# Optimization experiments

Measured on AMD Instinct MI355X. Metric: run time of the kernel, lower is better.

The kernel has to match this reference:

```python
import jax, jax.numpy as jnp
import numpy as np

NUM_OBJECTS = 6          # self.NUM_OBJECTS
SCORE_THRESH = 1e-4      # self.score_tresh
NMS_THRESHS = jnp.asarray(np.arange(0.001, 1.0, 0.1), dtype=jnp.float32)  # 10 thresholds
K_CAND = 1024            # fixed-shape cap on (proposal,class) candidates per image
CLASS_OFFSET = 4096.0    # > max image coord; batched_nms per-class offset trick


def _iou_matrix(b):
    # b: [K,4] xyxy -> [K,K] IoU
    x1, y1, x2, y2 = b[:, 0], b[:, 1], b[:, 2], b[:, 3]
    area = (x2 - x1) * (y2 - y1)
    iw = jnp.clip(jnp.minimum(x2[:, None], x2[None, :]) - jnp.maximum(x1[:, None], x1[None, :]), 0.0)
    ih = jnp.clip(jnp.minimum(y2[:, None], y2[None, :]) - jnp.maximum(y1[:, None], y1[None, :]), 0.0)
    inter = iw * ih
    union = area[:, None] + area[None, :] - inter
    return jnp.where(union > 0, inter / union, 0.0)


def _greedy_nms(iou, valid, thresh):
    # candidates are pre-sorted by descending score; sequential greedy suppression
    K = valid.shape[0]
    ar = jnp.arange(K)
    def body(i, keep):
        sup = keep[i] & (iou[i] > thresh) & (ar > i)
        return keep & ~sup
    return jax.lax.fori_loop(0, K, body, valid)


def _per_image(logits, boxes, feats, hw):
    # logits [N,81], boxes [N,80,4], feats [N,2048], hw [2] (h,w)
    C = boxes.shape[1]
    probs = jax.nn.softmax(logits, axis=-1)[:, :C]          # drop background class
    h = hw[0].astype(boxes.dtype)
    w = hw[1].astype(boxes.dtype)
    b = jnp.stack([jnp.clip(boxes[..., 0], 0.0, w),         # clip to image
                   jnp.clip(boxes[..., 1], 0.0, h),
                   jnp.clip(boxes[..., 2], 0.0, w),
                   jnp.clip(boxes[..., 3], 0.0, h)], axis=-1)
    scores = probs.reshape(-1)                              # [N*C]
    vals, idx = jax.lax.top_k(jnp.where(scores > SCORE_THRESH, scores, -1.0), K_CAND)
    cand_valid = vals > SCORE_THRESH
    cb = b.reshape(-1, 4)[idx]                              # [K,4]
    cls = (idx % C).astype(boxes.dtype)
    prop = idx // C                                         # proposal row index
    iou = _iou_matrix(cb + cls[:, None] * CLASS_OFFSET)     # per-class NMS via offsets
    keeps = jax.vmap(lambda t: _greedy_nms(iou, cand_valid, t))(NMS_THRESHS)  # [T,K]
    counts = keeps.sum(axis=1)
    # torch loop: break at first (smallest) thresh yielding len(ids)==6, i.e. >=6 kept
    ok = counts >= NUM_OBJECTS
    t_sel = jnp.where(jnp.any(ok), jnp.argmax(ok), NMS_THRESHS.shape[0] - 1)
    keep = keeps[t_sel]
    _, top = jax.lax.top_k(jnp.where(keep, vals, -jnp.inf), NUM_OBJECTS)
    ids = prop[top]                                         # [6]
    return feats[ids].T                                     # [2048, 6] (permute(1,0))


def _forward(cls_logits, boxes, feature_pooled, image_hw):
    return jax.vmap(_per_image)(cls_logits, boxes, feature_pooled, image_hw)  # [B,2048,6]


def setup_inputs() -> dict:
    key = jax.random.key(0)
    k1, k2, k3, k4, k5 = jax.random.split(key, 5)
    B, N, C, D = 8, 1000, 80, 2048
    cls_logits = jax.random.normal(k1, (B, N, C + 1), dtype=jnp.float32)
    ctr = jax.random.uniform(k2, (B, N, C, 2), minval=0.0, maxval=800.0)
    sz = jax.random.uniform(k3, (B, N, C, 2), minval=8.0, maxval=200.0)
    boxes = jnp.concatenate([ctr - sz * 0.5, ctr + sz * 0.5], axis=-1).astype(jnp.float32)
    feature_pooled = jax.random.normal(k4, (B, N, D), dtype=jnp.float32)
    image_hw = jax.random.randint(k5, (B, 2), 600, 800, dtype=jnp.int32)
    return {"cls_logits": cls_logits, "boxes": boxes,
            "feature_pooled": feature_pooled, "image_hw": image_hw}


def reference(cls_logits, boxes, feature_pooled, image_hw):
    return _forward(cls_logits, boxes, feature_pooled, image_hw)
```

## Files before the change

### kernel.cpp

```cpp
#include <hip/hip_runtime.h>
#include <cmath>
#include <cstdint>

#define NB 8
#define NPROP 1000
#define NCLS 80
#define NLOG 81
#define KCAND 1024
#define NTH 10
#define DFEAT 2048
#define NOBJ 6
#define NSCORE (NPROP*NCLS)
#define HBLK 8
#define HCHUNK (NSCORE/HBLK)
#define PCHUNK (NPROP/HBLK)
#define CCAP 64

constexpr size_t OFF_SCORES = 0;
constexpr size_t SZ_SCORES  = (size_t)NB * NSCORE * 4;
constexpr size_t OFF_LISTA  = OFF_SCORES + SZ_SCORES;
constexpr size_t SZ_LISTA   = (size_t)NB * 20 * KCAND * 8;
constexpr size_t OFF_H1     = OFF_LISTA;
constexpr size_t OFF_H2     = OFF_H1 + (size_t)NB * HBLK * 2048 * 4;
constexpr size_t OFF_PIV    = OFF_H2 + (size_t)NB * HBLK * 2048 * 4;
constexpr size_t OFF_CBUF   = OFF_PIV + (size_t)NB * 8 * 4;
constexpr size_t OFF_CANDK  = OFF_LISTA + SZ_LISTA;
constexpr size_t SZ_CANDK   = (size_t)NB * KCAND * 8;
constexpr size_t OFF_CX1    = OFF_CANDK + SZ_CANDK;
constexpr size_t SZ_CARR    = (size_t)NB * KCAND * 4;
constexpr size_t OFF_CY1    = OFF_CX1 + SZ_CARR;
constexpr size_t OFF_CX2    = OFF_CY1 + SZ_CARR;
constexpr size_t OFF_CY2    = OFF_CX2 + SZ_CARR;
constexpr size_t OFF_CAREA  = OFF_CY2 + SZ_CARR;
constexpr size_t OFF_CPROP  = OFF_CAREA + SZ_CARR;
constexpr size_t OFF_VALIDW = OFF_CPROP + SZ_CARR;
constexpr size_t SZ_VALIDW  = (size_t)NB * 16 * 8;
constexpr size_t OFF_CCNT   = OFF_VALIDW + SZ_VALIDW;
constexpr size_t OFF_CLIST  = OFF_CCNT + (size_t)NB * NCLS * 4;
constexpr size_t OFF_KEEPS  = OFF_CLIST + (size_t)NB * NCLS * CCAP * 4;
constexpr size_t SZ_KEEPS   = (size_t)NB * NTH * 16 * 8;

__device__ __forceinline__ float nms_th(int t) {
    return (float)(0.001 + 0.1 * (double)t);
}

__device__ __forceinline__ unsigned score_vkey(float v) {
    float vv = (v > 1e-4f) ? v : -1.0f;
    unsigned bits = __float_as_uint(vv);
    unsigned u = (bits & 0x80000000u) ? ~bits : (bits | 0x80000000u);
    return ~u;
}

__global__ __launch_bounds__(1024) void k_softhist(const float* __restrict__ logits,
                                                   float* __restrict__ scores,
                                                   unsigned* __restrict__ hist1) {
    __shared__ unsigned hh[2048];
    int img = blockIdx.x >> 3, blk = blockIdx.x & 7;
    int tid = threadIdx.x, wid = tid >> 6, lane = tid & 63;
    hh[tid] = 0; hh[tid + 1024] = 0;
    __syncthreads();
    for (int p = wid; p < PCHUNK; p += 16) {
        int prop = blk * PCHUNK + p;
        const float* L = logits + ((size_t)img * NPROP + prop) * NLOG;
        float l0 = L[lane];
        float l1 = (lane < 17) ? L[64 + lane] : -INFINITY;
        float m = fmaxf(l0, l1);
        #pragma unroll
        for (int o = 32; o > 0; o >>= 1) m = fmaxf(m, __shfl_xor(m, o, 64));
        float e0 = expf(l0 - m);
        float e1 = (lane < 17) ? expf(l1 - m) : 0.f;
        float s = e0 + e1;
        #pragma unroll
        for (int o = 32; o > 0; o >>= 1) s += __shfl_xor(s, o, 64);
        float* op = scores + ((size_t)img * NPROP + prop) * NCLS;
        float p0 = e0 / s;
        op[lane] = p0;
        atomicAdd(&hh[score_vkey(p0) >> 21], 1u);
        if (lane < 16) {
            float p1 = e1 / s;
            op[64 + lane] = p1;
            atomicAdd(&hh[score_vkey(p1) >> 21], 1u);
        }
    }
    __syncthreads();
    unsigned* outp = hist1 + ((size_t)img * HBLK + blk) * 2048;
    outp[tid] = hh[tid];
    outp[tid + 1024] = hh[tid + 1024];
}

__device__ __forceinline__ void pivot_scan(const unsigned* __restrict__ h8, unsigned K,
                                           int* __restrict__ out_b, int* __restrict__ out_rem) {
    __shared__ unsigned wsum[16];
    int tid = threadIdx.x;
    unsigned a = 0, b = 0;
    #pragma unroll
    for (int s = 0; s < HBLK; ++s) {
        a += h8[s * 2048 + 2 * tid];
        b += h8[s * 2048 + 2 * tid + 1];
    }
    unsigned p = a + b;
    unsigned x = p;
    #pragma unroll
    for (int d = 1; d < 64; d <<= 1) {
        unsigned y = __shfl_up(x, (unsigned)d, 64);
        if ((tid & 63) >= d) x += y;
    }
    if ((tid & 63) == 63) wsum[tid >> 6] = x;
    __syncthreads();
    if (tid < 16) {
        unsigned w = wsum[tid];
        #pragma unroll
        for (int d = 1; d < 16; d <<= 1) {
            unsigned y = __shfl_up(w, (unsigned)d, 64);
            if (tid >= d) w += y;
        }
        wsum[tid] = w;
    }
    __syncthreads();
    unsigned wex = (tid >= 64) ? wsum[(tid >> 6) - 1] : 0u;
    unsigned incl = x + wex;
    unsigned E = incl - p;
    if (E < K && E + a >= K)              { *out_b = 2 * tid;     *out_rem = (int)(K - E); }
    else if (E + a < K && E + a + b >= K) { *out_b = 2 * tid + 1; *out_rem = (int)(K - (E + a)); }
}

__global__ __launch_bounds__(1024) void k_hist2p(const float* __restrict__ scores,
                                                 const unsigned* __restrict__ hist1,
                                                 unsigned* __restrict__ hist2,
                                                 int* __restrict__ piv) {
    __shared__ unsigned hh[2048];
    __shared__ int sb, sr;
    int img = blockIdx.x >> 3, blk = blockIdx.x & 7;
    int tid = threadIdx.x;
    hh[tid] = 0; hh[tid + 1024] = 0;
    pivot_scan(hist1 + (size_t)img * HBLK * 2048, KCAND, &sb, &sr);
    __syncthreads();
    unsigned b1 = (unsigned)sb;
    const float* sc = scores + (size_t)img * NSCORE + (size_t)blk * HCHUNK;
    for (int e = tid; e < HCHUNK; e += 1024) {
        unsigned vk = score_vkey(sc[e]);
        if ((vk >> 21) == b1) atomicAdd(&hh[(vk >> 10) & 2047u], 1u);
    }
    __syncthreads();
    unsigned* outp = hist2 + ((size_t)img * HBLK + blk) * 2048;
    outp[tid] = hh[tid];
    outp[tid + 1024] = hh[tid + 1024];
    if (blk == 0 && tid == 0) {
        piv[img * 8 + 0] = sb;
        piv[img * 8 + 1] = sr;
        piv[img * 8 + 3] = 0;
    }
}

__global__ __launch_bounds__(1024) void k_gatherp(const float* __restrict__ scores,
                                                  const unsigned* __restrict__ hist2,
                                                  int* __restrict__ piv,
                                                  unsigned long long* __restrict__ cbuf,
                                                  int* __restrict__ ccnt,
                                                  unsigned long long* __restrict__ validw,
                                                  unsigned long long* __restrict__ keeps) {
    __shared__ int sb2, sr2;
    __shared__ unsigned lcnt, gbase;
    int img = blockIdx.x >> 3, blk = blockIdx.x & 7;
    int tid = threadIdx.x;
    if (blockIdx.x == 0) {
        if (tid < NB * NCLS) ccnt[tid] = 0;
        if (tid >= 640 && tid < 640 + NB * 16) validw[tid - 640] = 0ULL;
    }
    if (blockIdx.x == 1) {
        for (int k = tid; k < NB * NTH * 16; k += 1024) keeps[k] = 0ULL;
    }
    if (tid == 0) lcnt = 0;
    unsigned K2 = (unsigned)piv[img * 8 + 1];
    pivot_scan(hist2 + (size_t)img * HBLK * 2048, K2, &sb2, &sr2);
    __syncthreads();
    unsigned T22 = ((unsigned)piv[img * 8 + 0] << 11) | (unsigned)sb2;
    const float* sc = scores + (size_t)img * NSCORE + (size_t)blk * HCHUNK;
    unsigned long long sel[(HCHUNK + 1023) / 1024];
    int ns = 0;
    for (int e = tid; e < HCHUNK; e += 1024) {
        unsigned vk = score_vkey(sc[e]);
        if ((vk >> 10) <= T22)
            sel[ns++] = ((unsigned long long)vk << 32) | (unsigned)(blk * HCHUNK + e);
    }
    unsigned lp = atomicAdd(&lcnt, (unsigned)ns);
    __syncthreads();
    if (tid == 0) gbase = atomicAdd((unsigned*)&piv[img * 8 + 3], lcnt);
    __syncthreads();
    unsigned long long* ob = cbuf + (size_t)img * 2048;
    for (int i = 0; i < ns; ++i) {
        unsigned pos = gbase + lp + (unsigned)i;
        if (pos < 2048) ob[pos] = sel[i];
    }
}

__global__ __launch_bounds__(256) void k_rankcand(const unsigned long long* __restrict__ cbuf,
                                                  const int* __restrict__ piv,
                                                  const float* __restrict__ boxes,
                                                  const int* __restrict__ hw,
                                                  float* __restrict__ cx1, float* __restrict__ cy1,
                                                  float* __restrict__ cx2, float* __restrict__ cy2,
                                                  float* __restrict__ car, int* __restrict__ cprop,
                                                  unsigned long long* __restrict__ validw,
                                                  int* __restrict__ ccnt, int* __restrict__ clist) {
    __shared__ unsigned long long keys[2048];
    int img = blockIdx.x >> 3, sl = blockIdx.x & 7;
    int tid = threadIdx.x;
    int cnt = piv[img * 8 + 3]; if (cnt > 2048) cnt = 2048;
    const unsigned long long* ib = cbuf + (size_t)img * 2048;
    #pragma unroll
    for (int k = 0; k < 8; ++k) {
        int t = k * 256 + tid;
        keys[t] = (t < cnt) ? ib[t] : ~0ULL;
    }
    __syncthreads();
    unsigned long long a = keys[sl * 256 + tid];
    int r = 0;
    #pragma unroll 8
    for (int j = 0; j < cnt; ++j) r += (keys[j] < a) ? 1 : 0;
    if (sl * 256 + tid < cnt && r < KCAND) {
        unsigned u   = ~(unsigned)(a >> 32);
        unsigned idx = (unsigned)a;
        const unsigned uth = __float_as_uint(1e-4f) | 0x80000000u;
        bool valid = u > uth;
        int prop = (int)(idx / NCLS);
        int cls  = (int)(idx - (unsigned)prop * NCLS);
        const float4 bx = *(const float4*)(boxes + ((((size_t)img * NPROP + prop) * NCLS + cls) << 2));
        float h = (float)hw[img * 2 + 0];
        float w = (float)hw[img * 2 + 1];
        float x1 = fminf(fmaxf(bx.x, 0.f), w);
        float y1 = fminf(fmaxf(bx.y, 0.f), h);
        float x2 = fminf(fmaxf(bx.z, 0.f), w);
        float y2 = fminf(fmaxf(bx.w, 0.f), h);
        float offc = __fmul_rn((float)cls, 4096.0f);
        x1 = __fadd_rn(x1, offc); y1 = __fadd_rn(y1, offc);
        x2 = __fadd_rn(x2, offc); y2 = __fadd_rn(y2, offc);
        float area = __fmul_rn(__fsub_rn(x2, x1), __fsub_rn(y2, y1));
        int o = img * KCAND + r;
        cx1[o] = x1; cy1[o] = y1; cx2[o] = x2; cy2[o] = y2;
        car[o] = area; cprop[o] = prop;
        if (valid) atomicOr(&validw[img * 16 + (r >> 6)], 1ULL << (r & 63));
        int slot = atomicAdd(&ccnt[img * NCLS + cls], 1);
        if (slot < CCAP) clist[(img * NCLS + cls) * CCAP + slot] = r;
    }
}

__global__ __launch_bounds__(256) void k_cnms(const int* __restrict__ ccnt,
                                              const int* __restrict__ clist,
                                              const float* __restrict__ cx1,
                                              const float* __restrict__ cy1,
                                              const float* __restrict__ cx2,
                                              const float* __restrict__ cy2,
                                              const float* __restrict__ car,
                                              const unsigned long long* __restrict__ validw,
                                              unsigned long long* __restrict__ keeps) {
    int gid  = blockIdx.x * 4 + (threadIdx.x >> 6);
    int lane = threadIdx.x & 63;
    if (gid >= NB * NCLS) return;
    int img = gid / NCLS, cls = gid - img * NCLS;
    int n = ccnt[img * NCLS + cls];
    if (n > CCAP) n = CCAP;
    if (n == 0) return;
    int r = (lane < n) ? clist[(img * NCLS + cls) * CCAP + lane] : 0x7fffffff;
    int pos = 0;
    for (int j = 0; j < n; ++j) {
        int rj = __shfl(r, j, 64);
        pos += (rj < r) ? 1 : 0;
    }
    int srt = 0;
    for (int j = 0; j < n; ++j) {
        int pj = __shfl(pos, j, 64);
        int rj = __shfl(r, j, 64);
        if (pj == lane) srt = rj;
    }
    bool act = lane < n;
    int base = img * KCAND;
    float x1 = 0, y1 = 0, x2 = 0, y2 = 0, ar = 0;
    bool val = false;
    if (act) {
        x1 = cx1[base + srt]; y1 = cy1[base + srt];
        x2 = cx2[base + srt]; y2 = cy2[base + srt]; ar = car[base + srt];
        val = (validw[img * 16 + (srt >> 6)] >> (srt & 63)) & 1ULL;
    }
    unsigned long long m[NTH];
    #pragma unroll
    for (int t = 0; t < NTH; ++t) m[t] = 0ULL;
    for (int b = 0; b < n; ++b) {
        float xj1 = __shfl(x1, b, 64), yj1 = __shfl(y1, b, 64);
        float xj2 = __shfl(x2, b, 64), yj2 = __shfl(y2, b, 64);
        float aj  = __shfl(ar, b, 64);
        float iw = fmaxf(__fsub_rn(fminf(x2, xj2), fmaxf(x1, xj1)), 0.f);
        float ih = fmaxf(__fsub_rn(fminf(y2, yj2), fmaxf(y1, yj1)), 0.f);
        float inter = __fmul_rn(iw, ih);
        float uni   = __fsub_rn(__fadd_rn(ar, aj), inter);
        float iou   = (uni > 0.f) ? __fdiv_rn(inter, uni) : 0.f;
        if (act && b < lane) {
            #pragma unroll
            for (int t = 0; t < NTH; ++t)
                if (iou > nms_th(t)) m[t] |= 1ULL << b;
        }
    }
    unsigned long long vmask = __ballot(act && val);
    for (int t = 0; t < NTH; ++t) {
        unsigned long long keep = vmask;
        for (int it = 0; it <= n; ++it) {
            bool nk = act && val && ((m[t] & keep) == 0ULL);
            unsigned long long nb = __ballot(nk);
            if (nb == keep) break;
            keep = nb;
        }
        if (act && ((keep >> lane) & 1ULL))
            atomicOr(&keeps[((size_t)img * NTH + t) * 16 + (srt >> 6)], 1ULL << (srt & 63));
    }
}

__global__ __launch_bounds__(256) void k_selfeat(const unsigned long long* __restrict__ keeps,
                                                 const int* __restrict__ cprop,
                                                 const float* __restrict__ feats,
                                                 float* __restrict__ outp) {
    __shared__ int scnt[NTH];
    __shared__ unsigned long long skw[16];
    __shared__ int stsel;
    __shared__ int sids[NOBJ];
    int img = blockIdx.x >> 3;
    int tid = threadIdx.x;
    if (tid < NTH) scnt[tid] = 0;
    __syncthreads();
    if (tid < NTH * 16) {
        unsigned long long w = keeps[(size_t)img * NTH * 16 + tid];
        int pc = __popcll(w);
        if (pc) atomicAdd(&scnt[tid >> 4], pc);
    }
    __syncthreads();
    if (tid == 0) {
        int tsel = NTH - 1;
        for (int t = 0; t < NTH; ++t) if (scnt[t] >= NOBJ) { tsel = t; break; }
        stsel = tsel;
    }
    __syncthreads();
    if (tid < 16) skw[tid] = keeps[((size_t)img * NTH + stsel) * 16 + tid];
    __syncthreads();
    if (tid == 0) {
        int got = 0;
        for (int k = 0; k < 16 && got < NOBJ; ++k) {
            unsigned long long x = skw[k];
            while (x && got < NOBJ) {
                int b = __builtin_ctzll(x);
                sids[got++] = cprop[img * KCAND + k * 64 + b];
                x &= x - 1;
            }
        }
        for (int k = 0; k < 16 && got < NOBJ; ++k) {
            unsigned long long x = ~skw[k];
            while (x && got < NOBJ) {
                int b = __builtin_ctzll(x);
                sids[got++] = cprop[img * KCAND + k * 64 + b];
                x &= x - 1;
            }
        }
    }
    __syncthreads();
    int d = (blockIdx.x & 7) * 256 + tid;
    const float* fb = feats + (size_t)img * NPROP * DFEAT;
    float* ob = outp + ((size_t)img * DFEAT + d) * NOBJ;
    #pragma unroll
    for (int s = 0; s < NOBJ; ++s)
        ob[s] = fb[(size_t)sids[s] * DFEAT + d];
}

extern "C" void kernel_launch(void* const* d_in, const int* in_sizes, int n_in,
                              void* d_out, int out_size, void* d_ws, size_t ws_size,
                              hipStream_t stream) {
    const float* logits = (const float*)d_in[0];
    const float* boxes  = (const float*)d_in[1];
    const float* feats  = (const float*)d_in[2];
    const int*   hw     = (const int*)d_in[3];
    float* outp = (float*)d_out;

    char* ws = (char*)d_ws;
    float*              scores = (float*)(ws + OFF_SCORES);
    unsigned*           hist1  = (unsigned*)(ws + OFF_H1);
    unsigned*           hist2  = (unsigned*)(ws + OFF_H2);
    int*                piv    = (int*)(ws + OFF_PIV);
    unsigned long long* cbuf   = (unsigned long long*)(ws + OFF_CBUF);
    float* cx1 = (float*)(ws + OFF_CX1);
    float* cy1 = (float*)(ws + OFF_CY1);
    float* cx2 = (float*)(ws + OFF_CX2);
    float* cy2 = (float*)(ws + OFF_CY2);
    float* car = (float*)(ws + OFF_CAREA);
    int*   cprop = (int*)(ws + OFF_CPROP);
    unsigned long long* validw = (unsigned long long*)(ws + OFF_VALIDW);
    int*   ccnt  = (int*)(ws + OFF_CCNT);
    int*   clist = (int*)(ws + OFF_CLIST);
    unsigned long long* keeps  = (unsigned long long*)(ws + OFF_KEEPS);

    k_softhist<<<NB * HBLK, 1024, 0, stream>>>(logits, scores, hist1);
    k_hist2p<<<NB * HBLK, 1024, 0, stream>>>(scores, hist1, hist2, piv);
    k_gatherp<<<NB * HBLK, 1024, 0, stream>>>(scores, hist2, piv, cbuf, ccnt, validw, keeps);
    k_rankcand<<<NB * HBLK, 256, 0, stream>>>(cbuf, piv, boxes, hw,
                                              cx1, cy1, cx2, cy2, car, cprop,
                                              validw, ccnt, clist);
    k_cnms<<<(NB * NCLS + 3) / 4, 256, 0, stream>>>(ccnt, clist, cx1, cy1, cx2, cy2,
                                                    car, validw, keeps);
    k_selfeat<<<NB * HBLK, 256, 0, stream>>>(keeps, cprop, feats, outp);
}
```

Measured before the change: 163.6 us.

## Bucket-place candidates by histogram prefix sums to shrink rank computation

The gather kernel now recomputes both radix-histogram prefix scans and places each selected candidate directly into its bucket region using per-bucket atomic counters, so candidates arrive grouped by key range. The rank kernel then only compares each candidate against others in the same bucket instead of all up to 2048 gathered keys, dropping the shared-memory load and the O(n^2) count. Score reads in the histogram and gather passes are vectorised to float4. It adds global atomics per candidate, extra workspace for counters and prefixes, and defensive clamps on indices.

```diff
diff --git a/kernel.cpp b/kernel.cpp
--- a/kernel.cpp
+++ b/kernel.cpp
@@ -15,18 +15,17 @@
 #define HCHUNK (NSCORE/HBLK)
 #define PCHUNK (NPROP/HBLK)
 #define CCAP 64
+#define GMAX 2048
 
 constexpr size_t OFF_SCORES = 0;
-constexpr size_t SZ_SCORES  = (size_t)NB * NSCORE * 4;
-constexpr size_t OFF_LISTA  = OFF_SCORES + SZ_SCORES;
-constexpr size_t SZ_LISTA   = (size_t)NB * 20 * KCAND * 8;
-constexpr size_t OFF_H1     = OFF_LISTA;
+constexpr size_t OFF_H1     = OFF_SCORES + (size_t)NB * NSCORE * 4;
 constexpr size_t OFF_H2     = OFF_H1 + (size_t)NB * HBLK * 2048 * 4;
 constexpr size_t OFF_PIV    = OFF_H2 + (size_t)NB * HBLK * 2048 * 4;
 constexpr size_t OFF_CBUF   = OFF_PIV + (size_t)NB * 8 * 4;
-constexpr size_t OFF_CANDK  = OFF_LISTA + SZ_LISTA;
-constexpr size_t SZ_CANDK   = (size_t)NB * KCAND * 8;
-constexpr size_t OFF_CX1    = OFF_CANDK + SZ_CANDK;
+constexpr size_t OFF_GCNT   = OFF_CBUF + (size_t)NB * GMAX * 8;
+constexpr size_t OFF_S1P    = OFF_GCNT + (size_t)NB * 4096 * 4;
+constexpr size_t OFF_S2P    = OFF_S1P + (size_t)NB * 2048 * 4;
+constexpr size_t OFF_CX1    = OFF_S2P + (size_t)NB * 2048 * 4;
 constexpr size_t SZ_CARR    = (size_t)NB * KCAND * 4;
 constexpr size_t OFF_CY1    = OFF_CX1 + SZ_CARR;
 constexpr size_t OFF_CX2    = OFF_CY1 + SZ_CARR;
@@ -34,11 +33,9 @@
 constexpr size_t OFF_CAREA  = OFF_CY2 + SZ_CARR;
 constexpr size_t OFF_CPROP  = OFF_CAREA + SZ_CARR;
 constexpr size_t OFF_VALIDW = OFF_CPROP + SZ_CARR;
-constexpr size_t SZ_VALIDW  = (size_t)NB * 16 * 8;
-constexpr size_t OFF_CCNT   = OFF_VALIDW + SZ_VALIDW;
+constexpr size_t OFF_CCNT   = OFF_VALIDW + (size_t)NB * 16 * 8;
 constexpr size_t OFF_CLIST  = OFF_CCNT + (size_t)NB * NCLS * 4;
 constexpr size_t OFF_KEEPS  = OFF_CLIST + (size_t)NB * NCLS * CCAP * 4;
-constexpr size_t SZ_KEEPS   = (size_t)NB * NTH * 16 * 8;
 
 __device__ __forceinline__ float nms_th(int t) {
     return (float)(0.001 + 0.1 * (double)t);
@@ -49,6 +46,37 @@
     unsigned bits = __float_as_uint(vv);
     unsigned u = (bits & 0x80000000u) ? ~bits : (bits | 0x80000000u);
     return ~u;
+}
+
+__device__ __forceinline__ void scan2048(unsigned a, unsigned b, unsigned* pre,
+                                         unsigned K, int* out_b, int* out_rem) {
+    __shared__ unsigned wsum[16];
+    int tid = threadIdx.x;
+    unsigned p = a + b;
+    unsigned x = p;
+    #pragma unroll
+    for (int d = 1; d < 64; d <<= 1) {
+        unsigned y = __shfl_up(x, (unsigned)d, 64);
+        if ((tid & 63) >= d) x += y;
+    }
+    if ((tid & 63) == 63) wsum[tid >> 6] = x;
+    __syncthreads();
+    if (tid < 16) {
+        unsigned w = wsum[tid];
+        #pragma unroll
+        for (int d = 1; d < 16; d <<= 1) {
+            unsigned y = __shfl_up(w, (unsigned)d, 64);
+            if (tid >= d) w += y;
+        }
+        wsum[tid] = w;
+    }
+    __syncthreads();
+    unsigned wex = (tid >= 64) ? wsum[(tid >> 6) - 1] : 0u;
+    unsigned E = x + wex - p;
+    pre[2 * tid]     = E;
+    pre[2 * tid + 1] = E + a;
+    if (E < K && E + a >= K)              { *out_b = 2 * tid;     *out_rem = (int)(K - E); }
+    else if (E + a < K && E + a + b >= K) { *out_b = 2 * tid + 1; *out_rem = (int)(K - (E + a)); }
 }
 
 __global__ __launch_bounds__(1024) void k_softhist(const float* __restrict__ logits,
@@ -88,59 +116,40 @@
     outp[tid + 1024] = hh[tid + 1024];
 }
 
-__device__ __forceinline__ void pivot_scan(const unsigned* __restrict__ h8, unsigned K,
-                                           int* __restrict__ out_b, int* __restrict__ out_rem) {
-    __shared__ unsigned wsum[16];
-    int tid = threadIdx.x;
-    unsigned a = 0, b = 0;
-    #pragma unroll
-    for (int s = 0; s < HBLK; ++s) {
-        a += h8[s * 2048 + 2 * tid];
-        b += h8[s * 2048 + 2 * tid + 1];
-    }
-    unsigned p = a + b;
-    unsigned x = p;
-    #pragma unroll
-    for (int d = 1; d < 64; d <<= 1) {
-        unsigned y = __shfl_up(x, (unsigned)d, 64);
-        if ((tid & 63) >= d) x += y;
-    }
-    if ((tid & 63) == 63) wsum[tid >> 6] = x;
-    __syncthreads();
-    if (tid < 16) {
-        unsigned w = wsum[tid];
-        #pragma unroll
-        for (int d = 1; d < 16; d <<= 1) {
-            unsigned y = __shfl_up(w, (unsigned)d, 64);
-            if (tid >= d) w += y;
-        }
-        wsum[tid] = w;
-    }
-    __syncthreads();
-    unsigned wex = (tid >= 64) ? wsum[(tid >> 6) - 1] : 0u;
-    unsigned incl = x + wex;
-    unsigned E = incl - p;
-    if (E < K && E + a >= K)              { *out_b = 2 * tid;     *out_rem = (int)(K - E); }
-    else if (E + a < K && E + a + b >= K) { *out_b = 2 * tid + 1; *out_rem = (int)(K - (E + a)); }
-}
-
 __global__ __launch_bounds__(1024) void k_hist2p(const float* __restrict__ scores,
                                                  const unsigned* __restrict__ hist1,
                                                  unsigned* __restrict__ hist2,
-                                                 int* __restrict__ piv) {
+                                                 int* __restrict__ piv,
+                                                 unsigned* __restrict__ gcg) {
     __shared__ unsigned hh[2048];
     __shared__ int sb, sr;
     int img = blockIdx.x >> 3, blk = blockIdx.x & 7;
     int tid = threadIdx.x;
+    if (tid < 512) gcg[img * 4096 + blk * 512 + tid] = 0;
+    if (tid == 0) { sb = 0; sr = 1; }
+    __syncthreads();
+    {
+        unsigned a1 = 0, b1v = 0;
+        const unsigned* h1 = hist1 + (size_t)img * HBLK * 2048;
+        #pragma unroll
+        for (int s = 0; s < HBLK; ++s) {
+            a1  += h1[s * 2048 + 2 * tid];
+            b1v += h1[s * 2048 + 2 * tid + 1];
+        }
+        scan2048(a1, b1v, hh, KCAND, &sb, &sr);
+    }
+    __syncthreads();
     hh[tid] = 0; hh[tid + 1024] = 0;
-    pivot_scan(hist1 + (size_t)img * HBLK * 2048, KCAND, &sb, &sr);
-    __syncthreads();
-    unsigned b1 = (unsigned)sb;
-    const float* sc = scores + (size_t)img * NSCORE + (size_t)blk * HCHUNK;
-    for (int e = tid; e < HCHUNK; e += 1024) {
-        unsigned vk = score_vkey(sc[e]);
-        if ((vk >> 21) == b1) atomicAdd(&hh[(vk >> 10) & 2047u], 1u);
-    }
+    __syncthreads();
+    unsigned b1 = (unsigned)sb & 2047u;
+    const float4* sc4 = (const float4*)(scores + (size_t)img * NSCORE + (size_t)blk * HCHUNK);
+    #define H2S(val) { unsigned vk = score_vkey(val); \
+                       if ((vk >> 21) == b1) atomicAdd(&hh[(vk >> 10) & 2047u], 1u); }
+    for (int e4 = tid; e4 < HCHUNK / 4; e4 += 1024) {
+        float4 v = sc4[e4];
+        H2S(v.x) H2S(v.y) H2S(v.z) H2S(v.w)
+    }
+    #undef H2S
     __syncthreads();
     unsigned* outp = hist2 + ((size_t)img * HBLK + blk) * 2048;
     outp[tid] = hh[tid];
@@ -148,19 +157,23 @@
     if (blk == 0 && tid == 0) {
         piv[img * 8 + 0] = sb;
         piv[img * 8 + 1] = sr;
-        piv[img * 8 + 3] = 0;
     }
 }
 
 __global__ __launch_bounds__(1024) void k_gatherp(const float* __restrict__ scores,
+                                                  const unsigned* __restrict__ hist1,
                                                   const unsigned* __restrict__ hist2,
                                                   int* __restrict__ piv,
                                                   unsigned long long* __restrict__ cbuf,
+                                                  unsigned* __restrict__ gcg,
+                                                  unsigned* __restrict__ s1pg,
+                                                  unsigned* __restrict__ s2pg,
                                                   int* __restrict__ ccnt,
                                                   unsigned long long* __restrict__ validw,
                                                   unsigned long long* __restrict__ keeps) {
-    __shared__ int sb2, sr2;
-    __shared__ unsigned lcnt, gbase;
+    __shared__ unsigned s1p[2048];
+    __shared__ unsigned s2p[2048];
+    __shared__ int sb1, sr1, sb2, sr2;
     int img = blockIdx.x >> 3, blk = blockIdx.x & 7;
     int tid = threadIdx.x;
     if (blockIdx.x == 0) {
@@ -170,32 +183,64 @@
     if (blockIdx.x == 1) {
         for (int k = tid; k < NB * NTH * 16; k += 1024) keeps[k] = 0ULL;
     }
-    if (tid == 0) lcnt = 0;
-    unsigned K2 = (unsigned)piv[img * 8 + 1];
-    pivot_scan(hist2 + (size_t)img * HBLK * 2048, K2, &sb2, &sr2);
-    __syncthreads();
-    unsigned T22 = ((unsigned)piv[img * 8 + 0] << 11) | (unsigned)sb2;
-    const float* sc = scores + (size_t)img * NSCORE + (size_t)blk * HCHUNK;
-    unsigned long long sel[(HCHUNK + 1023) / 1024];
-    int ns = 0;
-    for (int e = tid; e < HCHUNK; e += 1024) {
-        unsigned vk = score_vkey(sc[e]);
-        if ((vk >> 10) <= T22)
-            sel[ns++] = ((unsigned long long)vk << 32) | (unsigned)(blk * HCHUNK + e);
-    }
-    unsigned lp = atomicAdd(&lcnt, (unsigned)ns);
-    __syncthreads();
-    if (tid == 0) gbase = atomicAdd((unsigned*)&piv[img * 8 + 3], lcnt);
-    __syncthreads();
-    unsigned long long* ob = cbuf + (size_t)img * 2048;
-    for (int i = 0; i < ns; ++i) {
-        unsigned pos = gbase + lp + (unsigned)i;
-        if (pos < 2048) ob[pos] = sel[i];
+    if (tid == 0) { sb1 = 0; sr1 = 1; sb2 = 0; sr2 = 1; }
+    __syncthreads();
+    {
+        unsigned a1 = 0, b1v = 0;
+        const unsigned* h1 = hist1 + (size_t)img * HBLK * 2048;
+        #pragma unroll
+        for (int s = 0; s < HBLK; ++s) {
+            a1  += h1[s * 2048 + 2 * tid];
+            b1v += h1[s * 2048 + 2 * tid + 1];
+        }
+        scan2048(a1, b1v, s1p, KCAND, &sb1, &sr1);
+    }
+    __syncthreads();
+    {
+        unsigned a2 = 0, b2v = 0;
+        const unsigned* h2 = hist2 + (size_t)img * HBLK * 2048;
+        #pragma unroll
+        for (int s = 0; s < HBLK; ++s) {
+            a2  += h2[s * 2048 + 2 * tid];
+            b2v += h2[s * 2048 + 2 * tid + 1];
+        }
+        scan2048(a2, b2v, s2p, (unsigned)sr1, &sb2, &sr2);
+    }
+    __syncthreads();
+    unsigned b1 = (unsigned)sb1 & 2047u;
+    unsigned sb2m = (unsigned)sb2 & 2047u;
+    unsigned T22 = (b1 << 11) | sb2m;
+    const float4* sc4 = (const float4*)(scores + (size_t)img * NSCORE + (size_t)blk * HCHUNK);
+    unsigned long long* cb = cbuf + (size_t)img * GMAX;
+    unsigned* gc = gcg + img * 4096;
+    #define GAS(val, ei) { unsigned vk = score_vkey(val); unsigned t22 = vk >> 10; \
+        if (t22 <= T22) { \
+            unsigned h = vk >> 21; unsigned g, base; \
+            if (h == b1) { unsigned sub = t22 & 2047u; g = 2048u + sub; base = s1p[b1] + s2p[sub]; } \
+            else         { g = h;                      base = s1p[h]; } \
+            unsigned slot = atomicAdd(&gc[g], 1u); \
+            unsigned posn = base + slot; \
+            if (posn < GMAX) cb[posn] = ((unsigned long long)vk << 32) | (unsigned)(ei); } }
+    for (int e4 = tid; e4 < HCHUNK / 4; e4 += 1024) {
+        float4 v = sc4[e4];
+        int e = blk * HCHUNK + 4 * e4;
+        GAS(v.x, e) GAS(v.y, e + 1) GAS(v.z, e + 2) GAS(v.w, e + 3)
+    }
+    #undef GAS
+    if (blk == 0) {
+        s1pg[img * 2048 + tid] = s1p[tid];
+        s1pg[img * 2048 + tid + 1024] = s1p[tid + 1024];
+        s2pg[img * 2048 + tid] = s2p[tid];
+        s2pg[img * 2048 + tid + 1024] = s2p[tid + 1024];
+        if (tid == 0) piv[img * 8 + 4] = sb2;
     }
 }
 
 __global__ __launch_bounds__(256) void k_rankcand(const unsigned long long* __restrict__ cbuf,
                                                   const int* __restrict__ piv,
+                                                  const unsigned* __restrict__ gcg,
+                                                  const unsigned* __restrict__ s1pg,
+                                                  const unsigned* __restrict__ s2pg,
                                                   const float* __restrict__ boxes,
                                                   const int* __restrict__ hw,
                                                   float* __restrict__ cx1, float* __restrict__ cy1,
@@ -203,45 +248,61 @@
                                                   float* __restrict__ car, int* __restrict__ cprop,
                                                   unsigned long long* __restrict__ validw,
                                                   int* __restrict__ ccnt, int* __restrict__ clist) {
-    __shared__ unsigned long long keys[2048];
     int img = blockIdx.x >> 3, sl = blockIdx.x & 7;
     int tid = threadIdx.x;
-    int cnt = piv[img * 8 + 3]; if (cnt > 2048) cnt = 2048;
-    const unsigned long long* ib = cbuf + (size_t)img * 2048;
-    #pragma unroll
-    for (int k = 0; k < 8; ++k) {
-        int t = k * 256 + tid;
-        keys[t] = (t < cnt) ? ib[t] : ~0ULL;
-    }
-    __syncthreads();
-    unsigned long long a = keys[sl * 256 + tid];
-    int r = 0;
-    #pragma unroll 8
-    for (int j = 0; j < cnt; ++j) r += (keys[j] < a) ? 1 : 0;
-    if (sl * 256 + tid < cnt && r < KCAND) {
-        unsigned u   = ~(unsigned)(a >> 32);
-        unsigned idx = (unsigned)a;
-        const unsigned uth = __float_as_uint(1e-4f) | 0x80000000u;
-        bool valid = u > uth;
+    unsigned b1   = (unsigned)piv[img * 8 + 0] & 2047u;
+    unsigned sb2m = (unsigned)piv[img * 8 + 4] & 2047u;
+    const unsigned* s1p = s1pg + img * 2048;
+    const unsigned* s2p = s2pg + img * 2048;
+    const unsigned* gc  = gcg + img * 4096;
+    const unsigned long long* cb = cbuf + (size_t)img * GMAX;
+    int cnt = (int)(s1p[b1] + s2p[sb2m] + gc[2048u + sb2m]);
+    if (cnt > GMAX || cnt < 0) cnt = GMAX;
+    int p = sl * 256 + tid;
+    if (p < cnt) {
+        unsigned long long akey = cb[p];
+        unsigned vk = (unsigned)(akey >> 32);
+        unsigned h = vk >> 21;
+        unsigned base, gsz;
+        if (h == b1) {
+            unsigned sub = (vk >> 10) & 2047u;
+            base = s1p[b1] + s2p[sub];
+            gsz  = gc[2048u + sub];
+        } else {
+            base = s1p[h];
+            gsz  = gc[h];
+        }
+        unsigned r_ = base;
+        unsigned qe = base + gsz;
+        if (qe > (unsigned)GMAX) qe = (unsigned)GMAX;
+        for (unsigned q = base; q < qe; ++q)
+            r_ += (cb[q] < akey) ? 1u : 0u;
+        int r = (int)r_;
+        unsigned idx = (unsigned)akey;
         int prop = (int)(idx / NCLS);
-        int cls  = (int)(idx - (unsigned)prop * NCLS);
-        const float4 bx = *(const float4*)(boxes + ((((size_t)img * NPROP + prop) * NCLS + cls) << 2));
-        float h = (float)hw[img * 2 + 0];
-        float w = (float)hw[img * 2 + 1];
-        float x1 = fminf(fmaxf(bx.x, 0.f), w);
-        float y1 = fminf(fmaxf(bx.y, 0.f), h);
-        float x2 = fminf(fmaxf(bx.z, 0.f), w);
-        float y2 = fminf(fmaxf(bx.w, 0.f), h);
-        float offc = __fmul_rn((float)cls, 4096.0f);
-        x1 = __fadd_rn(x1, offc); y1 = __fadd_rn(y1, offc);
-        x2 = __fadd_rn(x2, offc); y2 = __fadd_rn(y2, offc);
-        float area = __fmul_rn(__fsub_rn(x2, x1), __fsub_rn(y2, y1));
-        int o = img * KCAND + r;
-        cx1[o] = x1; cy1[o] = y1; cx2[o] = x2; cy2[o] = y2;
-        car[o] = area; cprop[o] = prop;
-        if (valid) atomicOr(&validw[img * 16 + (r >> 6)], 1ULL << (r & 63));
-        int slot = atomicAdd(&ccnt[img * NCLS + cls], 1);
-        if (slot < CCAP) clist[(img * NCLS + cls) * CCAP + slot] = r;
+        if (r >= 0 && r < KCAND && (unsigned)prop < NPROP) {
+            unsigned u = ~vk;
+            const unsigned uth = __float_as_uint(1e-4f) | 0x80000000u;
+            bool valid = u > uth;
+            int cls = (int)(idx - (unsigned)prop * NCLS);
+            const float4 bx = *(const float4*)(boxes + ((((size_t)img * NPROP + prop) * NCLS + cls) << 2));
+            float fh = (float)hw[img * 2 + 0];
+            float fw = (float)hw[img * 2 + 1];
+            float x1 = fminf(fmaxf(bx.x, 0.f), fw);
+            float y1 = fminf(fmaxf(bx.y, 0.f), fh);
+            float x2 = fminf(fmaxf(bx.z, 0.f), fw);
+            float y2 = fminf(fmaxf(bx.w, 0.f), fh);
+            float offc = __fmul_rn((float)cls, 4096.0f);
+            x1 = __fadd_rn(x1, offc); y1 = __fadd_rn(y1, offc);
+            x2 = __fadd_rn(x2, offc); y2 = __fadd_rn(y2, offc);
+            float area = __fmul_rn(__fsub_rn(x2, x1), __fsub_rn(y2, y1));
+            int o = img * KCAND + r;
+            cx1[o] = x1; cy1[o] = y1; cx2[o] = x2; cy2[o] = y2;
+            car[o] = area; cprop[o] = prop;
+            if (valid) atomicOr(&validw[img * 16 + (r >> 6)], 1ULL << (r & 63));
+            int slot = atomicAdd(&ccnt[img * NCLS + cls], 1);
+            if (slot < CCAP) clist[(img * NCLS + cls) * CCAP + slot] = r;
+        }
     }
 }
 
@@ -273,6 +334,7 @@
         int rj = __shfl(r, j, 64);
         if (pj == lane) srt = rj;
     }
+    srt &= (KCAND - 1);
     bool act = lane < n;
     int base = img * KCAND;
     float x1 = 0, y1 = 0, x2 = 0, y2 = 0, ar = 0;
@@ -346,7 +408,8 @@
             unsigned long long x = skw[k];
             while (x && got < NOBJ) {
                 int b = __builtin_ctzll(x);
-                sids[got++] = cprop[img * KCAND + k * 64 + b];
+                int sid = cprop[img * KCAND + k * 64 + b];
+                sids[got++] = ((unsigned)sid < NPROP) ? sid : 0;
                 x &= x - 1;
             }
         }
@@ -354,7 +417,8 @@
             unsigned long long x = ~skw[k];
             while (x && got < NOBJ) {
                 int b = __builtin_ctzll(x);
-                sids[got++] = cprop[img * KCAND + k * 64 + b];
+                int sid = cprop[img * KCAND + k * 64 + b];
+                sids[got++] = ((unsigned)sid < NPROP) ? sid : 0;
                 x &= x - 1;
             }
         }
@@ -383,6 +447,9 @@
     unsigned*           hist2  = (unsigned*)(ws + OFF_H2);
     int*                piv    = (int*)(ws + OFF_PIV);
     unsigned long long* cbuf   = (unsigned long long*)(ws + OFF_CBUF);
+    unsigned*           gcg    = (unsigned*)(ws + OFF_GCNT);
+    unsigned*           s1pg   = (unsigned*)(ws + OFF_S1P);
+    unsigned*           s2pg   = (unsigned*)(ws + OFF_S2P);
     float* cx1 = (float*)(ws + OFF_CX1);
     float* cy1 = (float*)(ws + OFF_CY1);
     float* cx2 = (float*)(ws + OFF_CX2);
@@ -395,9 +462,10 @@
     unsigned long long* keeps  = (unsigned long long*)(ws + OFF_KEEPS);
 
     k_softhist<<<NB * HBLK, 1024, 0, stream>>>(logits, scores, hist1);
-    k_hist2p<<<NB * HBLK, 1024, 0, stream>>>(scores, hist1, hist2, piv);
-    k_gatherp<<<NB * HBLK, 1024, 0, stream>>>(scores, hist2, piv, cbuf, ccnt, validw, keeps);
-    k_rankcand<<<NB * HBLK, 256, 0, stream>>>(cbuf, piv, boxes, hw,
+    k_hist2p<<<NB * HBLK, 1024, 0, stream>>>(scores, hist1, hist2, piv, gcg);
+    k_gatherp<<<NB * HBLK, 1024, 0, stream>>>(scores, hist1, hist2, piv, cbuf,
+                                              gcg, s1pg, s2pg, ccnt, validw, keeps);
+    k_rankcand<<<NB * HBLK, 256, 0, stream>>>(cbuf, piv, gcg, s1pg, s2pg, boxes, hw,
                                               cx1, cy1, cx2, cy2, car, cprop,
                                               validw, ccnt, clist);
     k_cnms<<<(NB * NCLS + 3) / 4, 256, 0, stream>>>(ccnt, clist, cx1, cy1, cx2, cy2,
```

New measurement: 173.5 us. 6.0% more time.
